# Kernel optimization log

Measured on AMD Instinct MI355X. Metric: run time of the kernel, lower is better.

Reference implementation:

```python
import jax, jax.numpy as jnp
import numpy as np

B, T, C = 8, 4096, 1024
NH = 64          # module sets self.n_head = dim_head = 64
HD = C // NH     # 16


def setup_inputs() -> dict:
    key = jax.random.key(0)
    ks = jax.random.split(key, 9)
    s = 1.0 / np.sqrt(C).astype(np.float32)
    x = jax.random.normal(ks[0], (B, T, C), jnp.float32)
    Wq = jax.random.normal(ks[1], (C, C), jnp.float32) * s
    bq = jax.random.normal(ks[2], (C,), jnp.float32) * 0.01
    Wk = jax.random.normal(ks[3], (C, C), jnp.float32) * s
    bk = jax.random.normal(ks[4], (C,), jnp.float32) * 0.01
    Wv = jax.random.normal(ks[5], (C, C), jnp.float32) * s
    bv = jax.random.normal(ks[6], (C,), jnp.float32) * 0.01
    Wp = jax.random.normal(ks[7], (C, C), jnp.float32) * s
    bp = jax.random.normal(ks[8], (C,), jnp.float32) * 0.01
    return {"x": x, "Wq": Wq, "bq": bq, "Wk": Wk, "bk": bk,
            "Wv": Wv, "bv": bv, "Wp": Wp, "bp": bp}


def _heads(t):
    # [B, T, C] -> [B, NH, T, HD]
    return t.reshape(B, T, NH, HD).transpose(0, 2, 1, 3)


def reference(x, Wq, bq, Wk, bk, Wv, bv, Wp, bp):
    # self-attention path: y = x; kv_mask=None (masked path is unreachable in source)
    q = _heads(x @ Wq.T + bq)
    k = _heads(x @ Wk.T + bk)
    v = _heads(x @ Wv.T + bv)
    q = jax.nn.softmax(q, axis=-1)
    k = jax.nn.softmax(k, axis=-1)
    k_cumsum = k.sum(axis=2, keepdims=True)               # [B, NH, 1, HD]
    D_inv = 1.0 / (q * k_cumsum).sum(axis=-1, keepdims=True)  # [B, NH, T, 1]
    context = jnp.einsum('bhtd,bhte->bhde', k, v)          # [B, NH, HD, HD]
    y = jnp.einsum('bhtd,bhde->bhte', q, context) * D_inv  # [B, NH, T, HD]
    y = y.transpose(0, 2, 1, 3).reshape(B, T, C)           # b h n d -> b n (h d)
    return y @ Wp.T + bp
```

## Files before the change

kernel.cpp:

```cpp
#include <hip/hip_runtime.h>
#include <stdint.h>


typedef __attribute__((ext_vector_type(8))) __bf16 bf16x8;
typedef __attribute__((ext_vector_type(4))) float f32x4;
typedef __attribute__((ext_vector_type(4))) unsigned int u32x4;
typedef __attribute__((ext_vector_type(4))) unsigned short u16x4;

#define AS1 __attribute__((address_space(1)))
#define AS3 __attribute__((address_space(3)))

__device__ __forceinline__ unsigned short f2bf(float f) {
  unsigned int u = __builtin_bit_cast(unsigned int, f);
  u += 0x7FFFu + ((u >> 16) & 1u);
  return (unsigned short)(u >> 16);
}

__device__ __forceinline__ void gl_lds16(const unsigned short* g, unsigned short* l) {
  __builtin_amdgcn_global_load_lds((const AS1 unsigned int*)g, (AS3 unsigned int*)l, 16, 0, 0);
}

__global__ __launch_bounds__(256)
void cvt_x(const float* __restrict__ src, unsigned short* __restrict__ dst, int n4) {
  int i = blockIdx.x * blockDim.x + threadIdx.x;
  const int stride = gridDim.x * blockDim.x;
  for (; i < n4; i += stride) {
    f32x4 v = *(const f32x4*)(src + (size_t)i * 4);
    u16x4 o;
    o.x = f2bf(v.x); o.y = f2bf(v.y); o.z = f2bf(v.z); o.w = f2bf(v.w);
    *(u16x4*)(dst + (size_t)i * 4) = o;
  }
}

__global__ __launch_bounds__(256)
void cvt_w(const float* __restrict__ w0, const float* __restrict__ w1,
           const float* __restrict__ w2, const float* __restrict__ w3,
           unsigned short* __restrict__ dst) {
  const int g = blockIdx.x * 256 + threadIdx.x;
  const int w = g >> 17;
  const int r = g & 131071;
  const int f = r >> 6;
  const int l = r & 63;
  const int n = (f >> 5) * 16 + (l & 15);
  const int k = (f & 31) * 32 + (l >> 4) * 8;
  const float* ws[4] = {w0, w1, w2, w3};
  const float* src = ws[w] + (size_t)n * 1024 + k;
  f32x4 v0 = *(const f32x4*)src;
  f32x4 v1 = *(const f32x4*)(src + 4);
  u16x4 a, b;
  a.x = f2bf(v0.x); a.y = f2bf(v0.y); a.z = f2bf(v0.z); a.w = f2bf(v0.w);
  b.x = f2bf(v1.x); b.y = f2bf(v1.y); b.z = f2bf(v1.z); b.w = f2bf(v1.w);
  unsigned short* o = dst + (size_t)g * 8;
  *(u16x4*)o = a;
  *(u16x4*)(o + 4) = b;
}

template<int KIND>
__global__ __launch_bounds__(256, 3)
void gemm_pipe(const unsigned short* __restrict__ A,
               const unsigned short* __restrict__ Wf,
               const float* __restrict__ b0, const float* __restrict__ b1,
               const float* __restrict__ b2,
               unsigned short* __restrict__ oq, unsigned short* __restrict__ okT,
               unsigned short* __restrict__ ovT, float* __restrict__ of)
{
  __shared__ __align__(16) unsigned short lds[12288];

  const int tid  = threadIdx.x;
  const int lane = tid & 63;
  const int wid  = tid >> 6;

  const int flat  = blockIdx.x;
  const int xcd   = flat & 7;
  const int i     = flat >> 3;
  const int bcg   = i >> 8;
  const int r     = i & 255;
  const int panel = r >> 3;
  const int c     = r & 7;
  const int brow  = (xcd * 32 + panel) * 128;
  const int bcol  = (bcg * 8 + c) * 128;

  const int srow = wid * 16 + (lane >> 2);
  const int scol = ((lane & 3) ^ ((lane >> 3) & 3)) << 3;
  const unsigned short* a_src = A + (size_t)(brow + srow) * 1024 + scol;
  unsigned short* Ldst = lds + wid * 512;

  const int wm = (wid >> 1) * 64;
  const int wn = (wid & 1) * 64;
  const int fr = lane & 15;
  const int fg = lane >> 4;
  const int aoff = (wm + fr) * 32 + ((fg ^ ((fr >> 1) & 3)) << 3);

  const unsigned short* wfp = Wf + ((size_t)((bcol + wn) >> 4) * 32) * 512 + lane * 8;

  const f32x4 fz = {0.f, 0.f, 0.f, 0.f};
  f32x4 acc[4][4];
  #pragma unroll
  for (int mt = 0; mt < 4; ++mt)
    #pragma unroll
    for (int nt = 0; nt < 4; ++nt) acc[mt][nt] = fz;

  auto stage = [&](int t, int buf) {
    unsigned short* d = Ldst + buf * 4096;
    gl_lds16(a_src + t * 32, d);
    gl_lds16(a_src + t * 32 + 65536, d + 2048);
  };
  auto loadB = [&](int t, bf16x8 (&dst)[4]) {
    #pragma unroll
    for (int nt = 0; nt < 4; ++nt)
      dst[nt] = __builtin_bit_cast(bf16x8,
        *(const u32x4*)(wfp + (size_t)t * 512 + (size_t)nt * 16384));
  };

  bf16x8 brgA[4], brgB[4];

  loadB(0, brgA);
  stage(0, 0); stage(1, 1); stage(2, 2);
  asm volatile("s_waitcnt vmcnt(4)" ::: "memory");
  __builtin_amdgcn_sched_barrier(0);
  __builtin_amdgcn_s_barrier();

  auto body = [&](int t, bf16x8 (&bc_)[4], bf16x8 (&bn_)[4]) {
    const unsigned short* Lb = lds + (t % 3) * 4096;
    bf16x8 af[4];
    #pragma unroll
    for (int mt = 0; mt < 4; ++mt)
      af[mt] = __builtin_bit_cast(bf16x8, *(const u32x4*)&Lb[aoff + mt * 512]);
    asm volatile("s_waitcnt lgkmcnt(0)" ::: "memory");
    __builtin_amdgcn_sched_barrier(0);
    __builtin_amdgcn_s_barrier();
    if (t + 3 < 32) stage(t + 3, t % 3);
    if (t + 1 < 32) loadB(t + 1, bn_);
    if (t <= 28)      asm volatile("s_waitcnt vmcnt(6)" ::: "memory");
    else if (t <= 30) asm volatile("s_waitcnt vmcnt(4)" ::: "memory");
    else              asm volatile("s_waitcnt vmcnt(0)" ::: "memory");
    __builtin_amdgcn_sched_barrier(0);
    __builtin_amdgcn_s_setprio(1);
    #pragma unroll
    for (int mt = 0; mt < 4; ++mt)
      #pragma unroll
      for (int nt = 0; nt < 4; ++nt)
        acc[mt][nt] = __builtin_amdgcn_mfma_f32_16x16x32_bf16(af[mt], bc_[nt], acc[mt][nt], 0, 0, 0);
    __builtin_amdgcn_s_setprio(0);
  };

  for (int t = 0; t < 32; t += 2) {
    body(t,     brgA, brgB);
    body(t + 1, brgB, brgA);
  }

  const int sec = (KIND == 0) ? (bcol >> 10) : 0;
  const float* bias = (KIND == 1) ? b0 : (sec == 0 ? b0 : (sec == 1 ? b1 : b2));

  #pragma unroll
  for (int nt = 0; nt < 4; ++nt) {
    const int n_glob = bcol + wn + nt * 16 + fr;
    const int nn = (KIND == 0) ? (n_glob & 1023) : n_glob;
    const float bv = bias[nn];
    #pragma unroll
    for (int mt = 0; mt < 4; ++mt) {
      const int m0 = brow + wm + mt * 16 + fg * 4;
      float vals[4];
      #pragma unroll
      for (int r2 = 0; r2 < 4; ++r2) vals[r2] = acc[mt][nt][r2] + bv;

      if (KIND == 0 && sec <= 1) {
        #pragma unroll
        for (int r2 = 0; r2 < 4; ++r2) {
          float e = __expf(vals[r2]);
          float sm = e;
          #pragma unroll
          for (int s = 1; s < 16; s <<= 1) sm += __shfl_xor(sm, s, 64);
          vals[r2] = e * __builtin_amdgcn_rcpf(sm);
        }
      }

      if (KIND == 1) {
        #pragma unroll
        for (int r2 = 0; r2 < 4; ++r2)
          of[(size_t)(m0 + r2) * 1024 + n_glob] = vals[r2];
      } else if (sec == 0) {
        #pragma unroll
        for (int r2 = 0; r2 < 4; ++r2)
          oq[(size_t)(m0 + r2) * 1024 + nn] = f2bf(vals[r2]);
      } else {
        unsigned short* o = (sec == 1) ? okT : ovT;
        const int bb = m0 >> 12;
        const int t0 = m0 & 4095;
        const int hh = nn >> 4;
        const int dd = nn & 15;
        u16x4 pk;
        pk.x = f2bf(vals[0]); pk.y = f2bf(vals[1]);
        pk.z = f2bf(vals[2]); pk.w = f2bf(vals[3]);
        *(u16x4*)&o[(((size_t)bb * 64 + hh) * 16 + dd) * 4096 + t0] = pk;
      }
    }
  }
}

__global__ __launch_bounds__(256)
void attn_kernel(const unsigned short* __restrict__ qb,
                 const unsigned short* __restrict__ kT,
                 const unsigned short* __restrict__ vT,
                 unsigned short* __restrict__ yb)
{
  const int head = blockIdx.x;
  const int tid  = threadIdx.x;
  const int lane = tid & 63;
  const int wid  = tid >> 6;
  const int fr   = lane & 15;
  const int fg   = lane >> 4;

  const unsigned short* kTh = kT + (size_t)head * 16 * 4096;
  const unsigned short* vTh = vT + (size_t)head * 16 * 4096;

  const u32x4 uz = {0u, 0u, 0u, 0u};
  const f32x4 fz = {0.f, 0.f, 0.f, 0.f};
  const u32x4 uo = {0x3F803F80u, 0x3F803F80u, 0x3F803F80u, 0x3F803F80u};
  const bf16x8 ones = __builtin_bit_cast(bf16x8, uo);

  f32x4 cctx = fz, ckc = fz;
  #pragma unroll 4
  for (int t0 = wid * 1024; t0 < (wid + 1) * 1024; t0 += 32) {
    bf16x8 ak = __builtin_bit_cast(bf16x8, *(const u32x4*)&kTh[(size_t)fr * 4096 + t0 + fg * 8]);
    bf16x8 bv = __builtin_bit_cast(bf16x8, *(const u32x4*)&vTh[(size_t)fr * 4096 + t0 + fg * 8]);
    cctx = __builtin_amdgcn_mfma_f32_16x16x32_bf16(ak, bv, cctx, 0, 0, 0);
    ckc  = __builtin_amdgcn_mfma_f32_16x16x32_bf16(ak, ones, ckc, 0, 0, 0);
  }

  __shared__ float red[4][16][16];
  __shared__ float kcr[4][16];
  __shared__ float ctxf[16][16];
  __shared__ float kcf[16];

  #pragma unroll
  for (int r = 0; r < 4; ++r) red[wid][fg * 4 + r][fr] = cctx[r];
  if (fr == 0) {
    #pragma unroll
    for (int r = 0; r < 4; ++r) kcr[wid][fg * 4 + r] = ckc[r];
  }
  __syncthreads();
  {
    const int d = tid >> 4, e = tid & 15;
    ctxf[d][e] = red[0][d][e] + red[1][d][e] + red[2][d][e] + red[3][d][e];
    if (tid < 16) kcf[tid] = kcr[0][tid] + kcr[1][tid] + kcr[2][tid] + kcr[3][tid];
  }
  __syncthreads();

  bf16x8 bctx = __builtin_bit_cast(bf16x8, uz);
  bf16x8 bkc  = __builtin_bit_cast(bf16x8, uz);
  if (fg < 2) {
    #pragma unroll
    for (int j = 0; j < 8; ++j) {
      const int d = fg * 8 + j;
      bctx[j] = (__bf16)ctxf[d][fr];
      bkc[j]  = (__bf16)kcf[d];
    }
  }

  const int b = head >> 6;
  const int h = head & 63;
  const size_t qbase = (size_t)b * 4096 * 1024 + (size_t)h * 16;

  for (int step = 0; step < 64; ++step) {
    const int t0 = step * 64 + wid * 16;
    bf16x8 af = __builtin_bit_cast(bf16x8, uz);
    if (fg < 2)
      af = __builtin_bit_cast(bf16x8, *(const u32x4*)&qb[qbase + (size_t)(t0 + fr) * 1024 + fg * 8]);
    f32x4 cy = __builtin_amdgcn_mfma_f32_16x16x32_bf16(af, bctx, fz, 0, 0, 0);
    f32x4 cd = __builtin_amdgcn_mfma_f32_16x16x32_bf16(af, bkc,  fz, 0, 0, 0);
    #pragma unroll
    for (int r = 0; r < 4; ++r) {
      const int t = t0 + fg * 4 + r;
      const float yv = cy[r] * __builtin_amdgcn_rcpf(cd[r]);
      yb[qbase + (size_t)t * 1024 + fr] = f2bf(yv);
    }
  }
}

extern "C" void kernel_launch(void* const* d_in, const int* in_sizes, int n_in,
                              void* d_out, int out_size, void* d_ws, size_t ws_size,
                              hipStream_t stream)
{
  (void)in_sizes; (void)n_in; (void)out_size; (void)ws_size;
  const float* x  = (const float*)d_in[0];
  const float* Wq = (const float*)d_in[1];
  const float* bq = (const float*)d_in[2];
  const float* Wk = (const float*)d_in[3];
  const float* bk = (const float*)d_in[4];
  const float* Wv = (const float*)d_in[5];
  const float* bv = (const float*)d_in[6];
  const float* Wp = (const float*)d_in[7];
  const float* bp = (const float*)d_in[8];

  char* ws = (char*)d_ws;
  unsigned short* xb  = (unsigned short*)(ws);
  unsigned short* wb  = (unsigned short*)(ws + 67108864);
  unsigned short* qb  = (unsigned short*)(ws + 75497472);
  unsigned short* kTb = (unsigned short*)(ws + 142606336);
  unsigned short* vTb = (unsigned short*)(ws + 209715200);

  cvt_x<<<2048, 256, 0, stream>>>(x, xb, 33554432 / 4);
  cvt_w<<<2048, 256, 0, stream>>>(Wq, Wk, Wv, Wp, wb);

  gemm_pipe<0><<<6144, 256, 0, stream>>>(xb, wb, bq, bk, bv, qb, kTb, vTb, nullptr);

  attn_kernel<<<512, 256, 0, stream>>>(qb, kTb, vTb, xb );

  gemm_pipe<1><<<2048, 256, 0, stream>>>(xb , wb + 3145728, bp, bp, bp,
                                         nullptr, nullptr, nullptr, (float*)d_out);
}
```

Before: 477.5 us.

## Process two heads per attention block to use full K=32 MFMA on Q

```diff
diff --git a/kernel.cpp b/kernel.cpp
--- a/kernel.cpp
+++ b/kernel.cpp
@@ -204,76 +204,107 @@
                  const unsigned short* __restrict__ vT,
                  unsigned short* __restrict__ yb)
 {
-  const int head = blockIdx.x;
+  const int pair = blockIdx.x;
+  const int b    = pair >> 5;
+  const int hp   = pair & 31;
   const int tid  = threadIdx.x;
   const int lane = tid & 63;
   const int wid  = tid >> 6;
   const int fr   = lane & 15;
   const int fg   = lane >> 4;
 
-  const unsigned short* kTh = kT + (size_t)head * 16 * 4096;
-  const unsigned short* vTh = vT + (size_t)head * 16 * 4096;
+  const unsigned short* kT0 = kT + ((size_t)(b * 64 + hp * 2) * 16) * 4096;
+  const unsigned short* vT0 = vT + ((size_t)(b * 64 + hp * 2) * 16) * 4096;
+  const unsigned short* kT1 = kT0 + 16 * 4096;
+  const unsigned short* vT1 = vT0 + 16 * 4096;
 
   const u32x4 uz = {0u, 0u, 0u, 0u};
   const f32x4 fz = {0.f, 0.f, 0.f, 0.f};
   const u32x4 uo = {0x3F803F80u, 0x3F803F80u, 0x3F803F80u, 0x3F803F80u};
   const bf16x8 ones = __builtin_bit_cast(bf16x8, uo);
 
-  f32x4 cctx = fz, ckc = fz;
-  #pragma unroll 4
+  f32x4 cctx0 = fz, ckc0 = fz, cctx1 = fz, ckc1 = fz;
+  #pragma unroll 2
   for (int t0 = wid * 1024; t0 < (wid + 1) * 1024; t0 += 32) {
-    bf16x8 ak = __builtin_bit_cast(bf16x8, *(const u32x4*)&kTh[(size_t)fr * 4096 + t0 + fg * 8]);
-    bf16x8 bv = __builtin_bit_cast(bf16x8, *(const u32x4*)&vTh[(size_t)fr * 4096 + t0 + fg * 8]);
-    cctx = __builtin_amdgcn_mfma_f32_16x16x32_bf16(ak, bv, cctx, 0, 0, 0);
-    ckc  = __builtin_amdgcn_mfma_f32_16x16x32_bf16(ak, ones, ckc, 0, 0, 0);
-  }
-
-  __shared__ float red[4][16][16];
-  __shared__ float kcr[4][16];
-  __shared__ float ctxf[16][16];
-  __shared__ float kcf[16];
+    const size_t off = (size_t)fr * 4096 + t0 + fg * 8;
+    bf16x8 ak0 = __builtin_bit_cast(bf16x8, *(const u32x4*)&kT0[off]);
+    bf16x8 bv0 = __builtin_bit_cast(bf16x8, *(const u32x4*)&vT0[off]);
+    bf16x8 ak1 = __builtin_bit_cast(bf16x8, *(const u32x4*)&kT1[off]);
+    bf16x8 bv1 = __builtin_bit_cast(bf16x8, *(const u32x4*)&vT1[off]);
+    cctx0 = __builtin_amdgcn_mfma_f32_16x16x32_bf16(ak0, bv0, cctx0, 0, 0, 0);
+    ckc0  = __builtin_amdgcn_mfma_f32_16x16x32_bf16(ak0, ones, ckc0, 0, 0, 0);
+    cctx1 = __builtin_amdgcn_mfma_f32_16x16x32_bf16(ak1, bv1, cctx1, 0, 0, 0);
+    ckc1  = __builtin_amdgcn_mfma_f32_16x16x32_bf16(ak1, ones, ckc1, 0, 0, 0);
+  }
+
+  __shared__ float red[4][2][16][16];
+  __shared__ float kcr[4][2][16];
+  __shared__ float ctxf[2][16][16];
+  __shared__ float kcf[2][16];
 
   #pragma unroll
-  for (int r = 0; r < 4; ++r) red[wid][fg * 4 + r][fr] = cctx[r];
+  for (int r = 0; r < 4; ++r) {
+    red[wid][0][fg * 4 + r][fr] = cctx0[r];
+    red[wid][1][fg * 4 + r][fr] = cctx1[r];
+  }
   if (fr == 0) {
     #pragma unroll
-    for (int r = 0; r < 4; ++r) kcr[wid][fg * 4 + r] = ckc[r];
+    for (int r = 0; r < 4; ++r) {
+      kcr[wid][0][fg * 4 + r] = ckc0[r];
+      kcr[wid][1][fg * 4 + r] = ckc1[r];
+    }
   }
   __syncthreads();
   {
-    const int d = tid >> 4, e = tid & 15;
-    ctxf[d][e] = red[0][d][e] + red[1][d][e] + red[2][d][e] + red[3][d][e];
-    if (tid < 16) kcf[tid] = kcr[0][tid] + kcr[1][tid] + kcr[2][tid] + kcr[3][tid];
+    const int h = tid >> 8;
+    (void)h;
+    const int d = (tid >> 4) & 15, e = tid & 15;
+    #pragma unroll
+    for (int hh = 0; hh < 2; ++hh)
+      ctxf[hh][d][e] = red[0][hh][d][e] + red[1][hh][d][e] + red[2][hh][d][e] + red[3][hh][d][e];
+    if (tid < 32) {
+      const int hh = tid >> 4, dd = tid & 15;
+      kcf[hh][dd] = kcr[0][hh][dd] + kcr[1][hh][dd] + kcr[2][hh][dd] + kcr[3][hh][dd];
+    }
   }
   __syncthreads();
 
-  bf16x8 bctx = __builtin_bit_cast(bf16x8, uz);
-  bf16x8 bkc  = __builtin_bit_cast(bf16x8, uz);
+  bf16x8 bctx0 = __builtin_bit_cast(bf16x8, uz);
+  bf16x8 bctx1 = __builtin_bit_cast(bf16x8, uz);
+  bf16x8 bkc0  = __builtin_bit_cast(bf16x8, uz);
+  bf16x8 bkc1  = __builtin_bit_cast(bf16x8, uz);
   if (fg < 2) {
     #pragma unroll
     for (int j = 0; j < 8; ++j) {
       const int d = fg * 8 + j;
-      bctx[j] = (__bf16)ctxf[d][fr];
-      bkc[j]  = (__bf16)kcf[d];
-    }
-  }
-
-  const int b = head >> 6;
-  const int h = head & 63;
-  const size_t qbase = (size_t)b * 4096 * 1024 + (size_t)h * 16;
+      bctx0[j] = (__bf16)ctxf[0][d][fr];
+      bkc0[j]  = (__bf16)kcf[0][d];
+    }
+  } else {
+    #pragma unroll
+    for (int j = 0; j < 8; ++j) {
+      const int d = (fg - 2) * 8 + j;
+      bctx1[j] = (__bf16)ctxf[1][d][fr];
+      bkc1[j]  = (__bf16)kcf[1][d];
+    }
+  }
+
+  const size_t cbase = (size_t)b * 4096 * 1024 + (size_t)hp * 32;
 
   for (int step = 0; step < 64; ++step) {
     const int t0 = step * 64 + wid * 16;
-    bf16x8 af = __builtin_bit_cast(bf16x8, uz);
-    if (fg < 2)
-      af = __builtin_bit_cast(bf16x8, *(const u32x4*)&qb[qbase + (size_t)(t0 + fr) * 1024 + fg * 8]);
-    f32x4 cy = __builtin_amdgcn_mfma_f32_16x16x32_bf16(af, bctx, fz, 0, 0, 0);
-    f32x4 cd = __builtin_amdgcn_mfma_f32_16x16x32_bf16(af, bkc,  fz, 0, 0, 0);
+    bf16x8 af = __builtin_bit_cast(bf16x8,
+        *(const u32x4*)&qb[cbase + (size_t)(t0 + fr) * 1024 + fg * 8]);
+    f32x4 cy0 = __builtin_amdgcn_mfma_f32_16x16x32_bf16(af, bctx0, fz, 0, 0, 0);
+    f32x4 cy1 = __builtin_amdgcn_mfma_f32_16x16x32_bf16(af, bctx1, fz, 0, 0, 0);
+    f32x4 cd0 = __builtin_amdgcn_mfma_f32_16x16x32_bf16(af, bkc0,  fz, 0, 0, 0);
+    f32x4 cd1 = __builtin_amdgcn_mfma_f32_16x16x32_bf16(af, bkc1,  fz, 0, 0, 0);
     #pragma unroll
     for (int r = 0; r < 4; ++r) {
       const int t = t0 + fg * 4 + r;
-      const float yv = cy[r] * __builtin_amdgcn_rcpf(cd[r]);
-      yb[qbase + (size_t)t * 1024 + fr] = f2bf(yv);
+      const size_t o = cbase + (size_t)t * 1024;
+      yb[o + fr]      = f2bf(cy0[r] * __builtin_amdgcn_rcpf(cd0[r]));
+      yb[o + 16 + fr] = f2bf(cy1[r] * __builtin_amdgcn_rcpf(cd1[r]));
     }
   }
 }
@@ -305,7 +336,7 @@
 
   gemm_pipe<0><<<6144, 256, 0, stream>>>(xb, wb, bq, bk, bv, qb, kTb, vTb, nullptr);
 
-  attn_kernel<<<512, 256, 0, stream>>>(qb, kTb, vTb, xb );
+  attn_kernel<<<256, 256, 0, stream>>>(qb, kTb, vTb, xb );
 
   gemm_pipe<1><<<2048, 256, 0, stream>>>(xb , wb + 3145728, bp, bp, bp,
                                          nullptr, nullptr, nullptr, (float*)d_out);
```

Measured after the change: 462.7 us. 3.1% less time.
